# Optimization experiments

Measured on AMD Instinct MI355X. Metric: run time of the kernel, lower is better.

The kernel has to match this reference:

```python
import jax, jax.numpy as jnp
import numpy as np

SINKHORN_ALPHA = 20.0
WEIGHT_LOSS_ECR = 100.0
OT_MAX_ITER = 100
STOP_THR = 0.005
EPS = 1e-16


def setup_inputs() -> dict:
    key = jax.random.key(0)
    # cost matrix: [num_topics, vocab]
    M = jax.random.uniform(key, (512, 65536), dtype=jnp.float32)
    return {"M": M}


def reference(M) -> jnp.ndarray:
    n, m = M.shape
    a = jnp.full((n, 1), 1.0 / n, dtype=M.dtype)   # row marginal
    b = jnp.full((m, 1), 1.0 / m, dtype=M.dtype)   # col marginal
    u0 = jnp.full((n, 1), 1.0 / n, dtype=M.dtype)
    K = jnp.exp(-M * SINKHORN_ALPHA)               # [n, m]

    def cond_fn(carry):
        u, v, err, cpt = carry
        return (err > STOP_THR) & (cpt < OT_MAX_ITER)

    def body_fn(carry):
        u, v, err, cpt = carry
        v = b / (K.T @ u + EPS)                    # [m, 1]
        u = a / (K @ v + EPS)                      # [n, 1]
        cpt = cpt + 1
        # convergence check every 50 iters (cpt % 50 == 1), matching torch loop
        err = jax.lax.cond(
            cpt % 50 == 1,
            lambda: jnp.sum(jnp.abs(v * (K.T @ u) - b)).astype(err.dtype),
            lambda: err,
        )
        return (u, v, err, cpt)

    init = (u0, jnp.zeros((m, 1), dtype=M.dtype), jnp.asarray(1.0, M.dtype), jnp.asarray(0, jnp.int32))
    u, v, _, _ = jax.lax.while_loop(cond_fn, body_fn, init)

    transp = u * (K * v.T)                         # [n, m] transport plan
    loss_ECR = jnp.sum(transp * M) * WEIGHT_LOSS_ECR
    return loss_ECR
```

## Files before the change

kernel.cpp:

```cpp
#include <hip/hip_runtime.h>
#include <hip/hip_cooperative_groups.h>

namespace cg = cooperative_groups;

#define NROW 512
#define NCOL 65536
#define BANDS 8
#define BPB   128

static __device__ __forceinline__ float wave_sum(float x) {
  #pragma unroll
  for (int off = 32; off; off >>= 1) x += __shfl_down(x, off, 64);
  return x;
}

__global__ __launch_bounds__(256)
void k1a_partial(const float* __restrict__ M, float* __restrict__ tPart,
                 float* __restrict__ eA) {
  const int tid = threadIdx.x, bid = blockIdx.x;
  const int band = bid >> 7, blk = bid & 127;
  const int chunk = tid & 127;
  const int part  = tid >> 7;
  const int col0  = (blk << 9) + (chunk << 2);
  const int r0    = (band << 6) + (part << 5);

  __shared__ float sCol[2 * 512];

  if (bid == 0 && tid < 3) eA[tid] = 0.f;

  float4 cs = {0.f, 0.f, 0.f, 0.f};
  #pragma unroll 8
  for (int r = r0; r < r0 + 32; ++r) {
    float4 m = *(const float4*)(M + (size_t)r * NCOL + col0);
    cs.x += __expf(-20.f * m.x);
    cs.y += __expf(-20.f * m.y);
    cs.z += __expf(-20.f * m.z);
    cs.w += __expf(-20.f * m.w);
  }
  *(float4*)(sCol + part * 512 + (chunk << 2)) = cs;
  __syncthreads();
  if (tid < 128) {
    float4 a = *(const float4*)(sCol + (tid << 2));
    float4 b = *(const float4*)(sCol + 512 + (tid << 2));
    float4 t = {a.x + b.x, a.y + b.y, a.z + b.z, a.w + b.w};
    *(float4*)(tPart + (size_t)band * NCOL + (blk << 9) + (tid << 2)) = t;
  }
}

__global__ __launch_bounds__(256)
void k1b_v1(const float* __restrict__ tPart, float* __restrict__ v) {
  const int gid = blockIdx.x * 256 + threadIdx.x;
  const int col0 = gid << 2;
  const float am = 1.0f / NROW, bm = 1.0f / NCOL, EPSV = 1e-16f;
  float4 t = {0.f, 0.f, 0.f, 0.f};
  #pragma unroll
  for (int b = 0; b < BANDS; ++b) {
    float4 p = *(const float4*)(tPart + (size_t)b * NCOL + col0);
    t.x += p.x; t.y += p.y; t.z += p.z; t.w += p.w;
  }
  float4 vv = {bm / (t.x * am + EPSV), bm / (t.y * am + EPSV),
               bm / (t.z * am + EPSV), bm / (t.w * am + EPSV)};
  *(float4*)(v + col0) = vv;
}

__global__ __launch_bounds__(256)
void k2_rowdot(const float* __restrict__ M, const float* __restrict__ v,
               float* __restrict__ u) {
  const int tid = threadIdx.x, row = blockIdx.x;
  const float am = 1.0f / NROW, EPSV = 1e-16f;
  const float4* M4 = (const float4*)M + (size_t)row * (NCOL / 4);
  const float4* V4 = (const float4*)v;
  __shared__ float sRed[4];

  float acc = 0.f;
  #pragma unroll 8
  for (int it = 0; it < NCOL / 4 / 256; ++it) {
    const int c = (it << 8) + tid;
    float4 m = M4[c];
    float4 vv = V4[c];
    acc += __expf(-20.f * m.x) * vv.x + __expf(-20.f * m.y) * vv.y
         + __expf(-20.f * m.z) * vv.z + __expf(-20.f * m.w) * vv.w;
  }
  acc = wave_sum(acc);
  if ((tid & 63) == 0) sRed[tid >> 6] = acc;
  __syncthreads();
  if (tid == 0)
    u[row] = am / (sRed[0] + sRed[1] + sRed[2] + sRed[3] + EPSV);
}

__global__ __launch_bounds__(256)
void k3a_partial(const float* __restrict__ M, const float* __restrict__ v,
                 const float* __restrict__ u, float* __restrict__ tPart,
                 float* __restrict__ eA) {
  const int tid = threadIdx.x, bid = blockIdx.x;
  const int band = bid >> 7, blk = bid & 127;
  const int chunk = tid & 127;
  const int part  = tid >> 7;
  const int col0  = (blk << 9) + (chunk << 2);
  const int r0l   = part << 5;

  __shared__ float sU[64];
  __shared__ float sCol[2 * 512];
  __shared__ float sRed[4];

  if (tid < 64) sU[tid] = u[(band << 6) + tid];
  __syncthreads();

  const float4 vv = *(const float4*)(v + col0);
  const float* Mb = M + (size_t)(band << 6) * NCOL;
  float4 cs = {0.f, 0.f, 0.f, 0.f};
  float lacc = 0.f;
  #pragma unroll 8
  for (int rl = r0l; rl < r0l + 32; ++rl) {
    float4 m = *(const float4*)(Mb + (size_t)rl * NCOL + col0);
    float e0 = __expf(-20.f * m.x), e1 = __expf(-20.f * m.y);
    float e2 = __expf(-20.f * m.z), e3 = __expf(-20.f * m.w);
    float us = sU[rl];
    cs.x = fmaf(e0, us, cs.x);
    cs.y = fmaf(e1, us, cs.y);
    cs.z = fmaf(e2, us, cs.z);
    cs.w = fmaf(e3, us, cs.w);
    lacc += us * (e0 * m.x * vv.x + e1 * m.y * vv.y
                + e2 * m.z * vv.z + e3 * m.w * vv.w);
  }
  *(float4*)(sCol + part * 512 + (chunk << 2)) = cs;
  lacc = wave_sum(lacc);
  if ((tid & 63) == 0) sRed[tid >> 6] = lacc;
  __syncthreads();
  if (tid < 128) {
    float4 a = *(const float4*)(sCol + (tid << 2));
    float4 b = *(const float4*)(sCol + 512 + (tid << 2));
    float4 t = {a.x + b.x, a.y + b.y, a.z + b.z, a.w + b.w};
    *(float4*)(tPart + (size_t)band * NCOL + (blk << 9) + (tid << 2)) = t;
  }
  if (tid == 0)
    atomicAdd(&eA[2], sRed[0] + sRed[1] + sRed[2] + sRed[3]);
}

__global__ __launch_bounds__(256)
void k3b_err(const float* __restrict__ tPart, const float* __restrict__ v,
             float* __restrict__ tArr, float* __restrict__ eA) {
  const int tid = threadIdx.x;
  const int gid = blockIdx.x * 256 + tid;
  const int col0 = gid << 2;
  const float bm = 1.0f / NCOL;
  __shared__ float sRed[4];

  float4 t = {0.f, 0.f, 0.f, 0.f};
  #pragma unroll
  for (int b = 0; b < BANDS; ++b) {
    float4 p = *(const float4*)(tPart + (size_t)b * NCOL + col0);
    t.x += p.x; t.y += p.y; t.z += p.z; t.w += p.w;
  }
  *(float4*)(tArr + col0) = t;
  float4 vv = *(const float4*)(v + col0);
  float pe = fabsf(vv.x * t.x - bm) + fabsf(vv.y * t.y - bm)
           + fabsf(vv.z * t.z - bm) + fabsf(vv.w * t.w - bm);
  pe = wave_sum(pe);
  if ((tid & 63) == 0) sRed[tid >> 6] = pe;
  __syncthreads();
  if (tid == 0)
    atomicAdd(&eA[0], sRed[0] + sRed[1] + sRed[2] + sRed[3]);
}

__global__ void k4_decide(const float* __restrict__ eA, float* __restrict__ out,
                          int* __restrict__ done) {
  if (threadIdx.x == 0) {
    if (eA[0] <= 0.005f) { out[0] = 100.f * eA[2]; done[0] = 1; }
    else                 { out[0] = 0.f;           done[0] = 0; }
  }
}

__global__ __launch_bounds__(1024)
void k5_fallback(const float* __restrict__ M, float* __restrict__ out,
                 float* __restrict__ v, float* __restrict__ u,
                 const float* __restrict__ tArr, float* __restrict__ eA,
                 const int* __restrict__ done) {
  if (done[0]) return;
  cg::grid_group grid = cg::this_grid();
  const int tid = threadIdx.x, bid = blockIdx.x;
  const float am = 1.0f / NROW, bm = 1.0f / NCOL, EPSV = 1e-16f;

  __shared__ float sU[NROW];
  __shared__ float sCol[16 * 256];
  __shared__ float sRedA[16], sRedB[16];

  const int chunk = tid & 63;
  const int part  = tid >> 6;
  const int col0  = (bid << 8) + (chunk << 2);
  const int r0    = part << 5;
  const int row0  = bid << 1;

  float tt = (tid < 256) ? tArr[(bid << 8) + tid] : 0.f;

  int cpt = 1;
  while (true) {
    if (tid < 256) v[(bid << 8) + tid] = bm / (tt + EPSV);
    grid.sync();
    cpt++;

    {
      const float4* M40 = (const float4*)M + (size_t)row0 * (NCOL / 4);
      const float4* M41 = (const float4*)M + (size_t)(row0 + 1) * (NCOL / 4);
      const float4* V4  = (const float4*)v;
      float ra = 0.f, rb = 0.f;
      #pragma unroll 4
      for (int it = 0; it < NCOL / 4 / 1024; ++it) {
        const int c = (it << 10) + tid;
        float4 vv = V4[c];
        float4 m0 = M40[c], m1 = M41[c];
        ra += __expf(-20.f * m0.x) * vv.x + __expf(-20.f * m0.y) * vv.y
            + __expf(-20.f * m0.z) * vv.z + __expf(-20.f * m0.w) * vv.w;
        rb += __expf(-20.f * m1.x) * vv.x + __expf(-20.f * m1.y) * vv.y
            + __expf(-20.f * m1.z) * vv.z + __expf(-20.f * m1.w) * vv.w;
      }
      ra = wave_sum(ra); rb = wave_sum(rb);
      if ((tid & 63) == 0) { sRedA[tid >> 6] = ra; sRedB[tid >> 6] = rb; }
      __syncthreads();
      if (tid < 2) {
        const float* sr = (tid == 0) ? sRedA : sRedB;
        float s = 0.f;
        #pragma unroll
        for (int w = 0; w < 16; ++w) s += sr[w];
        u[row0 + tid] = am / (s + EPSV);
      }
    }
    grid.sync();
    if (cpt >= 100) break;

    if (tid < NROW) sU[tid] = u[tid];
    __syncthreads();
    float4 cs = {0.f, 0.f, 0.f, 0.f};
    #pragma unroll 4
    for (int r = r0; r < r0 + 32; ++r) {
      float4 m = *(const float4*)(M + (size_t)r * NCOL + col0);
      float us = sU[r];
      cs.x = fmaf(__expf(-20.f * m.x), us, cs.x);
      cs.y = fmaf(__expf(-20.f * m.y), us, cs.y);
      cs.z = fmaf(__expf(-20.f * m.z), us, cs.z);
      cs.w = fmaf(__expf(-20.f * m.w), us, cs.w);
    }
    *(float4*)(sCol + part * 256 + (chunk << 2)) = cs;
    __syncthreads();
    if (tid < 256) {
      tt = 0.f;
      #pragma unroll
      for (int p = 0; p < 16; ++p) tt += sCol[p * 256 + tid];
    }

    if (cpt == 51) {
      float pe = (tid < 256) ? fabsf(v[(bid << 8) + tid] * tt - bm) : 0.f;
      pe = wave_sum(pe);
      __syncthreads();
      if ((tid & 63) == 0) sRedA[tid >> 6] = pe;
      __syncthreads();
      if (tid == 0) {
        float s = 0.f;
        #pragma unroll
        for (int w = 0; w < 16; ++w) s += sRedA[w];
        atomicAdd(&eA[1], s);
      }
      grid.sync();
      if (eA[1] <= 0.005f) break;
    }
  }

  __syncthreads();
  if (tid < NROW) sU[tid] = u[tid];
  __syncthreads();
  {
    const float4 vv = *(const float4*)(v + col0);
    float lacc = 0.f;
    #pragma unroll 4
    for (int r = r0; r < r0 + 32; ++r) {
      float4 m = *(const float4*)(M + (size_t)r * NCOL + col0);
      float us = sU[r];
      lacc += us * (__expf(-20.f * m.x) * m.x * vv.x
                  + __expf(-20.f * m.y) * m.y * vv.y
                  + __expf(-20.f * m.z) * m.z * vv.z
                  + __expf(-20.f * m.w) * m.w * vv.w);
    }
    lacc = wave_sum(lacc);
    if ((tid & 63) == 0) sRedA[tid >> 6] = lacc;
    __syncthreads();
    if (tid == 0) {
      float s = 0.f;
      #pragma unroll
      for (int w = 0; w < 16; ++w) s += sRedA[w];
      atomicAdd(out, 100.f * s);
    }
  }
}

extern "C" void kernel_launch(void* const* d_in, const int* in_sizes, int n_in,
                              void* d_out, int out_size, void* d_ws, size_t ws_size,
                              hipStream_t stream) {
  const float* M = (const float*)d_in[0];
  float* out = (float*)d_out;

  const size_t offV = 0;
  const size_t offT = offV + (size_t)NCOL * sizeof(float);
  const size_t offU = offT + (size_t)NCOL * sizeof(float);
  const size_t offE = offU + 4096;
  const size_t offD = offE + 256;
  const size_t offP = offD + 256;
  const size_t need = offP + (size_t)BANDS * NCOL * sizeof(float);
  if (ws_size < need) return;

  char* ws = (char*)d_ws;
  float* v     = (float*)(ws + offV);
  float* tArr  = (float*)(ws + offT);
  float* u     = (float*)(ws + offU);
  float* eA    = (float*)(ws + offE);
  int*   done  = (int*)(ws + offD);
  float* tPart = (float*)(ws + offP);

  k1a_partial<<<dim3(1024), dim3(256), 0, stream>>>(M, tPart, eA);
  k1b_v1     <<<dim3(64),   dim3(256), 0, stream>>>(tPart, v);
  k2_rowdot  <<<dim3(512),  dim3(256), 0, stream>>>(M, v, u);
  k3a_partial<<<dim3(1024), dim3(256), 0, stream>>>(M, v, u, tPart, eA);
  k3b_err    <<<dim3(64),   dim3(256), 0, stream>>>(tPart, v, tArr, eA);
  k4_decide  <<<dim3(1),    dim3(64),  0, stream>>>(eA, out, done);

  void* args[] = { (void*)&M, (void*)&out, (void*)&v, (void*)&u,
                   (void*)&tArr, (void*)&eA, (void*)&done };
  hipLaunchCooperativeKernel((void*)k5_fallback, dim3(256), dim3(1024),
                             args, 0, stream);
}
```

Baseline: 272.8 us.

## Split row-dot across four blocks per row and move loss to rowdot pass

The row-dot pass now splits each row into four column quarters, launching 2048 blocks instead of 512, and writes partial sums. The same pass also computes the loss-weighted partial sums, because it already reads M with the correct v. The second column-sum pass derives u from those partials and no longer computes the loss term, which removes its atomics and the per-element loss arithmetic. The column passes use 16 row bands with more explicit load unrolling, and the final decide kernel reduces the loss from the partials. The aim is better occupancy and fewer per-element ops, at the cost of larger workspace partial buffers and a 16-band reduction in the small kernels.

```diff
diff --git a/kernel.cpp b/kernel.cpp
--- a/kernel.cpp
+++ b/kernel.cpp
@@ -5,8 +5,7 @@
 
 #define NROW 512
 #define NCOL 65536
-#define BANDS 8
-#define BPB   128
+#define BANDS 16
 
 static __device__ __forceinline__ float wave_sum(float x) {
   #pragma unroll
@@ -14,28 +13,30 @@
   return x;
 }
 
-__global__ __launch_bounds__(256)
-void k1a_partial(const float* __restrict__ M, float* __restrict__ tPart,
-                 float* __restrict__ eA) {
+__global__ __launch_bounds__(256, 8)
+void p1_colsum(const float* __restrict__ M, float* __restrict__ t0Part,
+               float* __restrict__ eA) {
   const int tid = threadIdx.x, bid = blockIdx.x;
   const int band = bid >> 7, blk = bid & 127;
-  const int chunk = tid & 127;
-  const int part  = tid >> 7;
-  const int col0  = (blk << 9) + (chunk << 2);
-  const int r0    = (band << 6) + (part << 5);
+  const int chunk = tid & 127, part = tid >> 7;
+  const int col0 = (blk << 9) + (chunk << 2);
+  const int r0   = (band << 5) + (part << 4);
 
   __shared__ float sCol[2 * 512];
-
   if (bid == 0 && tid < 3) eA[tid] = 0.f;
 
+  const float* base = M + (size_t)r0 * NCOL + col0;
   float4 cs = {0.f, 0.f, 0.f, 0.f};
-  #pragma unroll 8
-  for (int r = r0; r < r0 + 32; ++r) {
-    float4 m = *(const float4*)(M + (size_t)r * NCOL + col0);
-    cs.x += __expf(-20.f * m.x);
-    cs.y += __expf(-20.f * m.y);
-    cs.z += __expf(-20.f * m.z);
-    cs.w += __expf(-20.f * m.w);
+  #pragma unroll
+  for (int rb = 0; rb < 16; rb += 4) {
+    float4 m0 = *(const float4*)(base + (size_t)(rb + 0) * NCOL);
+    float4 m1 = *(const float4*)(base + (size_t)(rb + 1) * NCOL);
+    float4 m2 = *(const float4*)(base + (size_t)(rb + 2) * NCOL);
+    float4 m3 = *(const float4*)(base + (size_t)(rb + 3) * NCOL);
+    cs.x += __expf(-20.f*m0.x) + __expf(-20.f*m1.x) + __expf(-20.f*m2.x) + __expf(-20.f*m3.x);
+    cs.y += __expf(-20.f*m0.y) + __expf(-20.f*m1.y) + __expf(-20.f*m2.y) + __expf(-20.f*m3.y);
+    cs.z += __expf(-20.f*m0.z) + __expf(-20.f*m1.z) + __expf(-20.f*m2.z) + __expf(-20.f*m3.z);
+    cs.w += __expf(-20.f*m0.w) + __expf(-20.f*m1.w) + __expf(-20.f*m2.w) + __expf(-20.f*m3.w);
   }
   *(float4*)(sCol + part * 512 + (chunk << 2)) = cs;
   __syncthreads();
@@ -43,136 +44,156 @@
     float4 a = *(const float4*)(sCol + (tid << 2));
     float4 b = *(const float4*)(sCol + 512 + (tid << 2));
     float4 t = {a.x + b.x, a.y + b.y, a.z + b.z, a.w + b.w};
-    *(float4*)(tPart + (size_t)band * NCOL + (blk << 9) + (tid << 2)) = t;
+    *(float4*)(t0Part + (size_t)band * NCOL + (blk << 9) + (tid << 2)) = t;
   }
 }
 
 __global__ __launch_bounds__(256)
-void k1b_v1(const float* __restrict__ tPart, float* __restrict__ v) {
-  const int gid = blockIdx.x * 256 + threadIdx.x;
-  const int col0 = gid << 2;
+void p1b_v1(const float* __restrict__ t0Part, float* __restrict__ v) {
+  const int col0 = (blockIdx.x * 256 + threadIdx.x) << 2;
   const float am = 1.0f / NROW, bm = 1.0f / NCOL, EPSV = 1e-16f;
   float4 t = {0.f, 0.f, 0.f, 0.f};
   #pragma unroll
   for (int b = 0; b < BANDS; ++b) {
-    float4 p = *(const float4*)(tPart + (size_t)b * NCOL + col0);
+    float4 p = *(const float4*)(t0Part + (size_t)b * NCOL + col0);
     t.x += p.x; t.y += p.y; t.z += p.z; t.w += p.w;
   }
-  float4 vv = {bm / (t.x * am + EPSV), bm / (t.y * am + EPSV),
-               bm / (t.z * am + EPSV), bm / (t.w * am + EPSV)};
+  float4 vv = {bm / (t.x*am + EPSV), bm / (t.y*am + EPSV),
+               bm / (t.z*am + EPSV), bm / (t.w*am + EPSV)};
   *(float4*)(v + col0) = vv;
 }
 
 __global__ __launch_bounds__(256)
-void k2_rowdot(const float* __restrict__ M, const float* __restrict__ v,
-               float* __restrict__ u) {
-  const int tid = threadIdx.x, row = blockIdx.x;
-  const float am = 1.0f / NROW, EPSV = 1e-16f;
-  const float4* M4 = (const float4*)M + (size_t)row * (NCOL / 4);
-  const float4* V4 = (const float4*)v;
-  __shared__ float sRed[4];
-
-  float acc = 0.f;
-  #pragma unroll 8
-  for (int it = 0; it < NCOL / 4 / 256; ++it) {
-    const int c = (it << 8) + tid;
-    float4 m = M4[c];
-    float4 vv = V4[c];
-    acc += __expf(-20.f * m.x) * vv.x + __expf(-20.f * m.y) * vv.y
-         + __expf(-20.f * m.z) * vv.z + __expf(-20.f * m.w) * vv.w;
-  }
-  acc = wave_sum(acc);
-  if ((tid & 63) == 0) sRed[tid >> 6] = acc;
-  __syncthreads();
-  if (tid == 0)
-    u[row] = am / (sRed[0] + sRed[1] + sRed[2] + sRed[3] + EPSV);
-}
-
-__global__ __launch_bounds__(256)
-void k3a_partial(const float* __restrict__ M, const float* __restrict__ v,
-                 const float* __restrict__ u, float* __restrict__ tPart,
-                 float* __restrict__ eA) {
+void p2_rowdot(const float* __restrict__ M, const float* __restrict__ v,
+               float* __restrict__ sPart, float* __restrict__ wPart) {
+  const int tid = threadIdx.x, bid = blockIdx.x;
+  const int row = bid >> 2, q = bid & 3;
+  const float4* M4 = (const float4*)M + (size_t)row * (NCOL/4) + q * 4096;
+  const float4* V4 = (const float4*)v + q * 4096;
+  __shared__ float sRed[8];
+
+  float s = 0.f, w = 0.f;
+  #pragma unroll
+  for (int it = 0; it < 16; it += 4) {
+    const int c0 = ((it + 0) << 8) + tid, c1 = ((it + 1) << 8) + tid;
+    const int c2 = ((it + 2) << 8) + tid, c3 = ((it + 3) << 8) + tid;
+    float4 m0 = M4[c0], m1 = M4[c1], m2 = M4[c2], m3 = M4[c3];
+    float4 v0 = V4[c0], v1 = V4[c1], v2 = V4[c2], v3 = V4[c3];
+    float4 e0 = {__expf(-20.f*m0.x), __expf(-20.f*m0.y), __expf(-20.f*m0.z), __expf(-20.f*m0.w)};
+    float4 e1 = {__expf(-20.f*m1.x), __expf(-20.f*m1.y), __expf(-20.f*m1.z), __expf(-20.f*m1.w)};
+    float4 e2 = {__expf(-20.f*m2.x), __expf(-20.f*m2.y), __expf(-20.f*m2.z), __expf(-20.f*m2.w)};
+    float4 e3 = {__expf(-20.f*m3.x), __expf(-20.f*m3.y), __expf(-20.f*m3.z), __expf(-20.f*m3.w)};
+    s += e0.x*v0.x + e0.y*v0.y + e0.z*v0.z + e0.w*v0.w
+       + e1.x*v1.x + e1.y*v1.y + e1.z*v1.z + e1.w*v1.w
+       + e2.x*v2.x + e2.y*v2.y + e2.z*v2.z + e2.w*v2.w
+       + e3.x*v3.x + e3.y*v3.y + e3.z*v3.z + e3.w*v3.w;
+    w += e0.x*m0.x*v0.x + e0.y*m0.y*v0.y + e0.z*m0.z*v0.z + e0.w*m0.w*v0.w
+       + e1.x*m1.x*v1.x + e1.y*m1.y*v1.y + e1.z*m1.z*v1.z + e1.w*m1.w*v1.w
+       + e2.x*m2.x*v2.x + e2.y*m2.y*v2.y + e2.z*m2.z*v2.z + e2.w*m2.w*v2.w
+       + e3.x*m3.x*v3.x + e3.y*m3.y*v3.y + e3.z*m3.z*v3.z + e3.w*m3.w*v3.w;
+  }
+  s = wave_sum(s); w = wave_sum(w);
+  if ((tid & 63) == 0) { sRed[tid >> 6] = s; sRed[4 + (tid >> 6)] = w; }
+  __syncthreads();
+  if (tid == 0) sPart[bid] = sRed[0] + sRed[1] + sRed[2] + sRed[3];
+  if (tid == 1) wPart[bid] = sRed[4] + sRed[5] + sRed[6] + sRed[7];
+}
+
+__global__ __launch_bounds__(256, 8)
+void p3_colsum2(const float* __restrict__ M, const float* __restrict__ sPart,
+                float* __restrict__ u, float* __restrict__ t2Part) {
   const int tid = threadIdx.x, bid = blockIdx.x;
   const int band = bid >> 7, blk = bid & 127;
-  const int chunk = tid & 127;
-  const int part  = tid >> 7;
-  const int col0  = (blk << 9) + (chunk << 2);
-  const int r0l   = part << 5;
-
-  __shared__ float sU[64];
+  const int chunk = tid & 127, part = tid >> 7;
+  const int col0 = (blk << 9) + (chunk << 2);
+  const int r0l  = part << 4;
+  const float am = 1.0f / NROW, EPSV = 1e-16f;
+
+  __shared__ float sU[32];
   __shared__ float sCol[2 * 512];
-  __shared__ float sRed[4];
-
-  if (tid < 64) sU[tid] = u[(band << 6) + tid];
-  __syncthreads();
-
-  const float4 vv = *(const float4*)(v + col0);
-  const float* Mb = M + (size_t)(band << 6) * NCOL;
+
+  if (tid < 32) {
+    const int i = (band << 5) + tid;
+    float s = sPart[4*i] + sPart[4*i+1] + sPart[4*i+2] + sPart[4*i+3];
+    float uv = am / (s + EPSV);
+    sU[tid] = uv;
+    if (blk == 0) u[i] = uv;
+  }
+  __syncthreads();
+
+  const float* base = M + (size_t)((band << 5) + r0l) * NCOL + col0;
   float4 cs = {0.f, 0.f, 0.f, 0.f};
-  float lacc = 0.f;
-  #pragma unroll 8
-  for (int rl = r0l; rl < r0l + 32; ++rl) {
-    float4 m = *(const float4*)(Mb + (size_t)rl * NCOL + col0);
-    float e0 = __expf(-20.f * m.x), e1 = __expf(-20.f * m.y);
-    float e2 = __expf(-20.f * m.z), e3 = __expf(-20.f * m.w);
-    float us = sU[rl];
-    cs.x = fmaf(e0, us, cs.x);
-    cs.y = fmaf(e1, us, cs.y);
-    cs.z = fmaf(e2, us, cs.z);
-    cs.w = fmaf(e3, us, cs.w);
-    lacc += us * (e0 * m.x * vv.x + e1 * m.y * vv.y
-                + e2 * m.z * vv.z + e3 * m.w * vv.w);
+  #pragma unroll
+  for (int rb = 0; rb < 16; rb += 4) {
+    float4 m0 = *(const float4*)(base + (size_t)(rb + 0) * NCOL);
+    float4 m1 = *(const float4*)(base + (size_t)(rb + 1) * NCOL);
+    float4 m2 = *(const float4*)(base + (size_t)(rb + 2) * NCOL);
+    float4 m3 = *(const float4*)(base + (size_t)(rb + 3) * NCOL);
+    float u0 = sU[r0l + rb], u1 = sU[r0l + rb + 1];
+    float u2 = sU[r0l + rb + 2], u3 = sU[r0l + rb + 3];
+    cs.x += __expf(-20.f*m0.x)*u0 + __expf(-20.f*m1.x)*u1 + __expf(-20.f*m2.x)*u2 + __expf(-20.f*m3.x)*u3;
+    cs.y += __expf(-20.f*m0.y)*u0 + __expf(-20.f*m1.y)*u1 + __expf(-20.f*m2.y)*u2 + __expf(-20.f*m3.y)*u3;
+    cs.z += __expf(-20.f*m0.z)*u0 + __expf(-20.f*m1.z)*u1 + __expf(-20.f*m2.z)*u2 + __expf(-20.f*m3.z)*u3;
+    cs.w += __expf(-20.f*m0.w)*u0 + __expf(-20.f*m1.w)*u1 + __expf(-20.f*m2.w)*u2 + __expf(-20.f*m3.w)*u3;
   }
   *(float4*)(sCol + part * 512 + (chunk << 2)) = cs;
-  lacc = wave_sum(lacc);
-  if ((tid & 63) == 0) sRed[tid >> 6] = lacc;
   __syncthreads();
   if (tid < 128) {
     float4 a = *(const float4*)(sCol + (tid << 2));
     float4 b = *(const float4*)(sCol + 512 + (tid << 2));
     float4 t = {a.x + b.x, a.y + b.y, a.z + b.z, a.w + b.w};
-    *(float4*)(tPart + (size_t)band * NCOL + (blk << 9) + (tid << 2)) = t;
-  }
-  if (tid == 0)
-    atomicAdd(&eA[2], sRed[0] + sRed[1] + sRed[2] + sRed[3]);
+    *(float4*)(t2Part + (size_t)band * NCOL + (blk << 9) + (tid << 2)) = t;
+  }
 }
 
 __global__ __launch_bounds__(256)
-void k3b_err(const float* __restrict__ tPart, const float* __restrict__ v,
-             float* __restrict__ tArr, float* __restrict__ eA) {
+void p4_err(const float* __restrict__ t2Part, const float* __restrict__ v,
+            float* __restrict__ t2, float* __restrict__ eA) {
   const int tid = threadIdx.x;
-  const int gid = blockIdx.x * 256 + tid;
-  const int col0 = gid << 2;
+  const int col0 = (blockIdx.x * 256 + tid) << 2;
   const float bm = 1.0f / NCOL;
   __shared__ float sRed[4];
 
   float4 t = {0.f, 0.f, 0.f, 0.f};
   #pragma unroll
   for (int b = 0; b < BANDS; ++b) {
-    float4 p = *(const float4*)(tPart + (size_t)b * NCOL + col0);
+    float4 p = *(const float4*)(t2Part + (size_t)b * NCOL + col0);
     t.x += p.x; t.y += p.y; t.z += p.z; t.w += p.w;
   }
-  *(float4*)(tArr + col0) = t;
+  *(float4*)(t2 + col0) = t;
   float4 vv = *(const float4*)(v + col0);
-  float pe = fabsf(vv.x * t.x - bm) + fabsf(vv.y * t.y - bm)
-           + fabsf(vv.z * t.z - bm) + fabsf(vv.w * t.w - bm);
+  float pe = fabsf(vv.x*t.x - bm) + fabsf(vv.y*t.y - bm)
+           + fabsf(vv.z*t.z - bm) + fabsf(vv.w*t.w - bm);
   pe = wave_sum(pe);
   if ((tid & 63) == 0) sRed[tid >> 6] = pe;
   __syncthreads();
-  if (tid == 0)
-    atomicAdd(&eA[0], sRed[0] + sRed[1] + sRed[2] + sRed[3]);
-}
-
-__global__ void k4_decide(const float* __restrict__ eA, float* __restrict__ out,
-                          int* __restrict__ done) {
-  if (threadIdx.x == 0) {
-    if (eA[0] <= 0.005f) { out[0] = 100.f * eA[2]; done[0] = 1; }
-    else                 { out[0] = 0.f;           done[0] = 0; }
+  if (tid == 0) atomicAdd(&eA[0], sRed[0] + sRed[1] + sRed[2] + sRed[3]);
+}
+
+__global__ __launch_bounds__(256)
+void p5_decide(const float* __restrict__ eA, const float* __restrict__ u,
+               const float* __restrict__ wPart, float* __restrict__ out,
+               int* __restrict__ done) {
+  const int tid = threadIdx.x;
+  __shared__ float sRed[4];
+  float l = 0.f;
+  #pragma unroll
+  for (int k = 0; k < 2; ++k) {
+    const int i = 2*tid + k;
+    l += u[i] * (wPart[4*i] + wPart[4*i+1] + wPart[4*i+2] + wPart[4*i+3]);
+  }
+  l = wave_sum(l);
+  if ((tid & 63) == 0) sRed[tid >> 6] = l;
+  __syncthreads();
+  if (tid == 0) {
+    float loss = 100.f * (sRed[0] + sRed[1] + sRed[2] + sRed[3]);
+    if (eA[0] <= 0.005f) { out[0] = loss; done[0] = 1; }
+    else                 { out[0] = 0.f;  done[0] = 0; }
   }
 }
 
 __global__ __launch_bounds__(1024)
-void k5_fallback(const float* __restrict__ M, float* __restrict__ out,
+void p6_fallback(const float* __restrict__ M, float* __restrict__ out,
                  float* __restrict__ v, float* __restrict__ u,
                  const float* __restrict__ tArr, float* __restrict__ eA,
                  const int* __restrict__ done) {
@@ -298,32 +319,38 @@
   const float* M = (const float*)d_in[0];
   float* out = (float*)d_out;
 
-  const size_t offV = 0;
-  const size_t offT = offV + (size_t)NCOL * sizeof(float);
-  const size_t offU = offT + (size_t)NCOL * sizeof(float);
-  const size_t offE = offU + 4096;
-  const size_t offD = offE + 256;
-  const size_t offP = offD + 256;
-  const size_t need = offP + (size_t)BANDS * NCOL * sizeof(float);
+  const size_t off0P = 0;
+  const size_t off2P = off0P + (size_t)BANDS * NCOL * sizeof(float);
+  const size_t offV  = off2P + (size_t)BANDS * NCOL * sizeof(float);
+  const size_t offT2 = offV  + (size_t)NCOL * sizeof(float);
+  const size_t offSP = offT2 + (size_t)NCOL * sizeof(float);
+  const size_t offWP = offSP + 8192;
+  const size_t offU  = offWP + 8192;
+  const size_t offEA = offU  + 2048;
+  const size_t offDN = offEA + 256;
+  const size_t need  = offDN + 256;
   if (ws_size < need) return;
 
   char* ws = (char*)d_ws;
-  float* v     = (float*)(ws + offV);
-  float* tArr  = (float*)(ws + offT);
-  float* u     = (float*)(ws + offU);
-  float* eA    = (float*)(ws + offE);
-  int*   done  = (int*)(ws + offD);
-  float* tPart = (float*)(ws + offP);
-
-  k1a_partial<<<dim3(1024), dim3(256), 0, stream>>>(M, tPart, eA);
-  k1b_v1     <<<dim3(64),   dim3(256), 0, stream>>>(tPart, v);
-  k2_rowdot  <<<dim3(512),  dim3(256), 0, stream>>>(M, v, u);
-  k3a_partial<<<dim3(1024), dim3(256), 0, stream>>>(M, v, u, tPart, eA);
-  k3b_err    <<<dim3(64),   dim3(256), 0, stream>>>(tPart, v, tArr, eA);
-  k4_decide  <<<dim3(1),    dim3(64),  0, stream>>>(eA, out, done);
+  float* t0Part = (float*)(ws + off0P);
+  float* t2Part = (float*)(ws + off2P);
+  float* v      = (float*)(ws + offV);
+  float* t2     = (float*)(ws + offT2);
+  float* sPart  = (float*)(ws + offSP);
+  float* wPart  = (float*)(ws + offWP);
+  float* u      = (float*)(ws + offU);
+  float* eA     = (float*)(ws + offEA);
+  int*   done   = (int*)(ws + offDN);
+
+  p1_colsum <<<dim3(2048), dim3(256), 0, stream>>>(M, t0Part, eA);
+  p1b_v1    <<<dim3(64),   dim3(256), 0, stream>>>(t0Part, v);
+  p2_rowdot <<<dim3(2048), dim3(256), 0, stream>>>(M, v, sPart, wPart);
+  p3_colsum2<<<dim3(2048), dim3(256), 0, stream>>>(M, sPart, u, t2Part);
+  p4_err    <<<dim3(64),   dim3(256), 0, stream>>>(t2Part, v, t2, eA);
+  p5_decide <<<dim3(1),    dim3(256), 0, stream>>>(eA, u, wPart, out, done);
 
   void* args[] = { (void*)&M, (void*)&out, (void*)&v, (void*)&u,
-                   (void*)&tArr, (void*)&eA, (void*)&done };
-  hipLaunchCooperativeKernel((void*)k5_fallback, dim3(256), dim3(1024),
+                   (void*)&t2, (void*)&eA, (void*)&done };
+  hipLaunchCooperativeKernel((void*)p6_fallback, dim3(256), dim3(1024),
                              args, 0, stream);
 }
```

Measured after the change: 274.7 us. No clear change (+0.7%).
